# Kernel tuning notes

Hardware: AMD Instinct MI355X
Metric: run time of the kernel (lower is better)

Reference implementation:

```python
import jax, jax.numpy as jnp
import numpy as np

N_SEGMENTS = 512  # number of superpoint segments (range of sptids)


def setup_inputs() -> dict:
    key = jax.random.key(0)
    k1, k2, k3, k4 = jax.random.split(key, 4)
    n, m, c = 32768, 16384, 21
    points = jax.random.normal(k1, (n, 3), dtype=jnp.float32)
    scores = jax.random.normal(k2, (n, c), dtype=jnp.float32)
    d_points = jax.random.normal(k3, (m, 3), dtype=jnp.float32)
    sptids = jax.random.randint(k4, (m,), 0, N_SEGMENTS, dtype=jnp.int32)
    return {"points": points, "scores": scores, "d_points": d_points, "sptids": sptids}


def reference(points, scores, d_points, sptids):
    # --- brute-force nearest neighbor for ALL downsampled points at once ---
    # squared euclidean distance; argmin is identical to torch.cdist's argmin
    d2 = (jnp.sum(d_points * d_points, axis=1, keepdims=True)
          + jnp.sum(points * points, axis=1)[None, :]
          - 2.0 * (d_points @ points.T))          # [m, n]
    nn_idx = jnp.argmin(d2, axis=1)               # [m]
    gathered = scores[nn_idx]                     # [m, C] == assign_features output

    # --- per-segment mean of gathered scores, then argmax -> segment label ---
    seg_sum = jax.ops.segment_sum(gathered, sptids, num_segments=N_SEGMENTS)  # [S, C]
    counts = jax.ops.segment_sum(jnp.ones(sptids.shape, gathered.dtype), sptids,
                                 num_segments=N_SEGMENTS)                      # [S]
    seg_mean = seg_sum / jnp.maximum(counts, 1.0)[:, None]
    seg_labels = jnp.argmax(seg_mean, axis=1)     # [S]
    labels = seg_labels[sptids][:, None].astype(jnp.int32)  # [m, 1], original index order

    # torch.cat of seg_points over sorted unique ids == stable sort of d_points by sptid
    order = jnp.argsort(sptids, stable=True)
    new_points = d_points[order]                  # [m, 3]
    return new_points, labels
```

## Files before the change

### kernel.cpp

```cpp
#include <hip/hip_runtime.h>
#include <cfloat>
#include <cstdint>

#define NSEG 512
#define C 21
#define PPB 512
#define EPS_PICK 1e-3f

typedef _Float16 half8 __attribute__((ext_vector_type(8)));
typedef float f32x16 __attribute__((ext_vector_type(16)));

__global__ __launch_bounds__(256, 4)
void k1_mfma_scatter(const float* __restrict__ pts, const float* __restrict__ dpts,
                     const int* __restrict__ sptids,
                     float4* __restrict__ pts4, float* __restrict__ pbvT,
                     int* __restrict__ segbase, int* __restrict__ sorted_orig,
                     float* __restrict__ out, int n, int m, int NCH)
{
    __shared__ half8 lbuf[1024];
    const int bid = blockIdx.x, t = threadIdx.x;

    if (bid < NCH) {
        int sb = bid;
        int* Hb   = (int*)lbuf;
        int* Ht   = Hb + NSEG;
        int* pair = Ht + NSEG;
        int* segs = pair + 256;
        Hb[t] = 0; Hb[t + 256] = 0; Ht[t] = 0; Ht[t + 256] = 0;
        __syncthreads();
        int before = sb * 256;
        for (int idx = t; idx < m; idx += 256) {
            int s = sptids[idx];
            atomicAdd(&Ht[s], 1);
            if (idx < before) atomicAdd(&Hb[s], 1);
        }
        __syncthreads();
        int e0 = Ht[2 * t], e1 = Ht[2 * t + 1];
        int v = e0 + e1;
        pair[t] = v;
        __syncthreads();
        for (int off = 1; off < 256; off <<= 1) {
            int add = (t >= off) ? pair[t - off] : 0;
            __syncthreads();
            v += add; pair[t] = v;
            __syncthreads();
        }
        int prev = (t > 0) ? pair[t - 1] : 0;
        int b0 = prev, b1 = prev + e0;
        if (sb == 0) { segbase[2 * t] = b0; segbase[2 * t + 1] = b1; }
        int hb0 = Hb[2 * t], hb1 = Hb[2 * t + 1];
        __syncthreads();
        Hb[2 * t] = b0 + hb0;
        Hb[2 * t + 1] = b1 + hb1;
        int i = sb * 256 + t;
        segs[t] = (i < m) ? sptids[i] : -1;
        __syncthreads();
        if (i < m) {
            int seg = segs[t];
            int rank = 0;
            for (int j = 0; j < t; j++) rank += (segs[j] == seg) ? 1 : 0;
            int pos = Hb[seg] + rank;
            out[pos * 3 + 0] = dpts[i * 3 + 0];
            out[pos * 3 + 1] = dpts[i * 3 + 1];
            out[pos * 3 + 2] = dpts[i * 3 + 2];
            sorted_orig[pos] = i;
        }
        return;
    }

    const int b2 = bid - NCH;
    const int qb = b2 & 31, pc = b2 >> 5;
    const int wave = t >> 6, lane = t & 63;
    const int g = lane >> 5, col = lane & 31;

    half8 bq[4];
#pragma unroll
    for (int k = 0; k < 4; k++) {
        int q = (qb * 16 + wave * 4 + k) * 32 + col;
        float b0 = dpts[q * 3 + 0], b1 = dpts[q * 3 + 1], b2c = dpts[q * 3 + 2];
        _Float16 bh0 = (_Float16)b0; _Float16 bl0 = (_Float16)(b0 - (float)bh0);
        _Float16 bh1 = (_Float16)b1; _Float16 bl1 = (_Float16)(b1 - (float)bh1);
        _Float16 bh2 = (_Float16)b2c; _Float16 bl2 = (_Float16)(b2c - (float)bh2);
        const _Float16 one = (_Float16)1.f, zz = (_Float16)0.f;
        half8 g0 = {bh0, bl0, bh0, bh1, bl1, bh1, bh2, bl2};
        half8 g1 = {bh2, one, one, zz, zz, zz, zz, zz};
        bq[k] = g ? g1 : g0;
    }

#pragma unroll
    for (int half = 0; half < 2; half++) {
        int j = half * 256 + t;
        int i = pc * PPB + j;
        float x = pts[i * 3 + 0], y = pts[i * 3 + 1], z = pts[i * 3 + 2];
        if (qb == 0)
            pts4[i] = make_float4(x, y, z, fmaf(x, x, fmaf(y, y, z * z)));
        float a0 = -2.f * x, a1 = -2.f * y, a2 = -2.f * z;
        _Float16 ah0 = (_Float16)a0; _Float16 al0 = (_Float16)(a0 - (float)ah0);
        _Float16 ah1 = (_Float16)a1; _Float16 al1 = (_Float16)(a1 - (float)ah1);
        _Float16 ah2 = (_Float16)a2; _Float16 al2 = (_Float16)(a2 - (float)ah2);
        double ps = (double)x * x + (double)y * y + (double)z * z;
        _Float16 s0 = (_Float16)(float)ps;
        double r1 = ps - (double)(float)s0;
        _Float16 s1 = (_Float16)(float)r1;
        half8 g0 = {ah0, ah0, al0, ah1, ah1, al1, ah2, ah2};
        half8 g1 = {al2, s0, s1, (_Float16)0.f, (_Float16)0.f,
                    (_Float16)0.f, (_Float16)0.f, (_Float16)0.f};
        int base = (j >> 5) * 64 + (j & 31) * 2;
        lbuf[base + 0] = g0;
        lbuf[base + 1] = g1;
    }
    __syncthreads();

    float run0 = FLT_MAX, run1 = FLT_MAX, run2 = FLT_MAX, run3 = FLT_MAX;
    const f32x16 zero = {0.f,0.f,0.f,0.f,0.f,0.f,0.f,0.f,0.f,0.f,0.f,0.f,0.f,0.f,0.f,0.f};
    const int aoff = col * 2 + g;

#pragma unroll 4
    for (int tt = 0; tt < 16; tt++) {
        half8 a = lbuf[tt * 64 + aoff];
        f32x16 c0 = __builtin_amdgcn_mfma_f32_32x32x16_f16(a, bq[0], zero, 0, 0, 0);
        f32x16 c1 = __builtin_amdgcn_mfma_f32_32x32x16_f16(a, bq[1], zero, 0, 0, 0);
        f32x16 c2 = __builtin_amdgcn_mfma_f32_32x32x16_f16(a, bq[2], zero, 0, 0, 0);
        f32x16 c3 = __builtin_amdgcn_mfma_f32_32x32x16_f16(a, bq[3], zero, 0, 0, 0);
#define FOLD(cc, rr)  { \
        float v = fminf(fminf(cc[0], cc[1]), cc[2]);   \
        v = fminf(fminf(v, cc[3]), cc[4]);             \
        v = fminf(fminf(v, cc[5]), cc[6]);             \
        v = fminf(fminf(v, cc[7]), cc[8]);             \
        v = fminf(fminf(v, cc[9]), cc[10]);            \
        v = fminf(fminf(v, cc[11]), cc[12]);           \
        v = fminf(fminf(v, cc[13]), cc[14]);           \
        rr = fminf(fminf(v, cc[15]), rr); }
        FOLD(c0, run0) FOLD(c1, run1) FOLD(c2, run2) FOLD(c3, run3)
#undef FOLD
    }

    {
        int qbase = (qb * 512 + wave * 128) * 64;
        float v0 = fminf(run0, __shfl_xor(run0, 32, 64));
        float v1 = fminf(run1, __shfl_xor(run1, 32, 64));
        float v2 = fminf(run2, __shfl_xor(run2, 32, 64));
        float v3 = fminf(run3, __shfl_xor(run3, 32, 64));
        if (lane < 32) {
            pbvT[(size_t)qbase + (0 * 32 + lane) * 64 + pc] = v0;
            pbvT[(size_t)qbase + (1 * 32 + lane) * 64 + pc] = v1;
            pbvT[(size_t)qbase + (2 * 32 + lane) * 64 + pc] = v2;
            pbvT[(size_t)qbase + (3 * 32 + lane) * 64 + pc] = v3;
        }
    }
}

__global__ __launch_bounds__(1024)
void k2_seg_pick(const float4* __restrict__ pts4, const float* __restrict__ dpts,
                 const float* __restrict__ scores, const float* __restrict__ pbvT,
                 const int* __restrict__ segbase, const int* __restrict__ sorted_orig,
                 float* __restrict__ out, int n, int m)
{
    __shared__ double wsum[16][C];
    __shared__ double total[C];
    __shared__ float lab;
    const int t = threadIdx.x, wave = t >> 6, lane = t & 63;
    const int s = blockIdx.x;
    const int base = segbase[s];
    const int end  = (s == NSEG - 1) ? m : segbase[s + 1];

    double acc = 0.0;
    for (int j = base + wave; j < end; j += 16) {
        int q = sorted_orig[j];
        float myv = pbvT[(size_t)q * 64 + lane];
        float g1 = myv;
#pragma unroll
        for (int off = 1; off < 64; off <<= 1) g1 = fminf(g1, __shfl_xor(g1, off, 64));
        float thr = g1 + EPS_PICK;
        unsigned long long msk = __ballot(myv <= thr);

        float fx = dpts[q * 3 + 0], fy = dpts[q * 3 + 1], fz = dpts[q * 3 + 2];
        float fm2x = -2.f * fx, fm2y = -2.f * fy, fm2z = -2.f * fz;
        double m2x = -2.0 * (double)fx, m2y = -2.0 * (double)fy, m2z = -2.0 * (double)fz;
        double best = 1e308; int bi = 0x7fffffff;
        while (msk) {
            int pc = __builtin_ctzll(msk); msk &= msk - 1;
            int pbase = pc * PPB + lane;
#pragma unroll
            for (int r2 = 0; r2 < PPB / 64; r2++) {
                int i = pbase + r2 * 64;
                if (i < n) {
                    float4 p = pts4[i];
                    float v = fmaf(p.x, fm2x, fmaf(p.y, fm2y, fmaf(p.z, fm2z, p.w)));
                    if (v <= thr) {
                        double ps = (double)p.x * p.x + (double)p.y * p.y + (double)p.z * p.z;
                        double dv = fma((double)p.x, m2x, fma((double)p.y, m2y,
                                    fma((double)p.z, m2z, ps)));
                        if (dv < best || (dv == best && i < bi)) { best = dv; bi = i; }
                    }
                }
            }
        }
#pragma unroll
        for (int off = 32; off; off >>= 1) {
            double ov = __shfl_down(best, off, 64);
            int oi = __shfl_down(bi, off, 64);
            if (ov < best || (ov == best && oi < bi)) { best = ov; bi = oi; }
        }
        int bi0 = __shfl(bi, 0, 64);
        if (lane < C)
            acc += (double)scores[(size_t)bi0 * C + lane];
    }
    if (lane < C) wsum[wave][lane] = acc;
    __syncthreads();
    if (t < C) {
        double tv = 0.0;
#pragma unroll
        for (int w = 0; w < 16; w++) tv += wsum[w][t];
        total[t] = tv;
    }
    __syncthreads();
    if (t == 0) {
        double bv = total[0]; int best = 0;
        for (int c = 1; c < C; c++)
            if (total[c] > bv) { bv = total[c]; best = c; }
        lab = (float)best;
    }
    __syncthreads();
    float fb = lab;
    for (int j = base + t; j < end; j += 1024)
        out[(size_t)m * 3 + sorted_orig[j]] = fb;
}

extern "C" void kernel_launch(void* const* d_in, const int* in_sizes, int n_in,
                              void* d_out, int out_size, void* d_ws, size_t ws_size,
                              hipStream_t stream) {
    const float* points = (const float*)d_in[0];
    const float* scores = (const float*)d_in[1];
    const float* dpts   = (const float*)d_in[2];
    const int*   sptids = (const int*)d_in[3];

    int n = in_sizes[0] / 3;
    int m = in_sizes[2] / 3;
    int NCH   = (m + 255) / 256;
    int QB    = (m + 511) / 512;
    int PCg   = (n + 511) / 512;
    int MFMAB = QB * PCg;

    char* ws = (char*)d_ws;
    float4* pts4        = (float4*)ws;  ws += (size_t)n * sizeof(float4);
    float*  pbvT        = (float*)ws;   ws += (size_t)m * 64 * sizeof(float);
    int*    segbase     = (int*)ws;     ws += (size_t)NSEG * sizeof(int);
    int*    sorted_orig = (int*)ws;     ws += (size_t)m * sizeof(int);

    k1_mfma_scatter<<<NCH + MFMAB, 256, 0, stream>>>(points, dpts, sptids,
                                                     pts4, pbvT, segbase, sorted_orig,
                                                     (float*)d_out, n, m, NCH);
    k2_seg_pick<<<NSEG, 1024, 0, stream>>>(pts4, dpts, scores, pbvT,
                                           segbase, sorted_orig, (float*)d_out, n, m);
}
```

Baseline: 49.11 us.

## Track best and second-best MFMA tile per chunk to narrow exact rescoring

```diff
diff --git a/kernel.cpp b/kernel.cpp
--- a/kernel.cpp
+++ b/kernel.cpp
@@ -6,6 +6,7 @@
 #define C 21
 #define PPB 512
 #define EPS_PICK 1e-3f
+#define SLACK 1.5e-4f
 
 typedef _Float16 half8 __attribute__((ext_vector_type(8)));
 typedef float f32x16 __attribute__((ext_vector_type(16)));
@@ -14,6 +15,7 @@
 void k1_mfma_scatter(const float* __restrict__ pts, const float* __restrict__ dpts,
                      const int* __restrict__ sptids,
                      float4* __restrict__ pts4, float* __restrict__ pbvT,
+                     unsigned* __restrict__ auxT,
                      int* __restrict__ segbase, int* __restrict__ sorted_orig,
                      float* __restrict__ out, int n, int m, int NCH)
 {
@@ -111,7 +113,10 @@
     }
     __syncthreads();
 
-    float run0 = FLT_MAX, run1 = FLT_MAX, run2 = FLT_MAX, run3 = FLT_MAX;
+    float run1[4], run2[4];
+    int ttix[4];
+#pragma unroll
+    for (int k = 0; k < 4; k++) { run1[k] = FLT_MAX; run2[k] = FLT_MAX; ttix[k] = 0; }
     const f32x16 zero = {0.f,0.f,0.f,0.f,0.f,0.f,0.f,0.f,0.f,0.f,0.f,0.f,0.f,0.f,0.f,0.f};
     const int aoff = col * 2 + g;
 
@@ -122,7 +127,7 @@
         f32x16 c1 = __builtin_amdgcn_mfma_f32_32x32x16_f16(a, bq[1], zero, 0, 0, 0);
         f32x16 c2 = __builtin_amdgcn_mfma_f32_32x32x16_f16(a, bq[2], zero, 0, 0, 0);
         f32x16 c3 = __builtin_amdgcn_mfma_f32_32x32x16_f16(a, bq[3], zero, 0, 0, 0);
-#define FOLD(cc, rr)  { \
+#define FOLD(cc, kk)  { \
         float v = fminf(fminf(cc[0], cc[1]), cc[2]);   \
         v = fminf(fminf(v, cc[3]), cc[4]);             \
         v = fminf(fminf(v, cc[5]), cc[6]);             \
@@ -130,22 +135,32 @@
         v = fminf(fminf(v, cc[9]), cc[10]);            \
         v = fminf(fminf(v, cc[11]), cc[12]);           \
         v = fminf(fminf(v, cc[13]), cc[14]);           \
-        rr = fminf(fminf(v, cc[15]), rr); }
-        FOLD(c0, run0) FOLD(c1, run1) FOLD(c2, run2) FOLD(c3, run3)
+        v = fminf(v, cc[15]);                          \
+        float nr2 = fminf(run2[kk], fmaxf(v, run1[kk])); \
+        if (v < run1[kk]) { ttix[kk] = tt; run1[kk] = v; } \
+        run2[kk] = nr2; }
+        FOLD(c0, 0) FOLD(c1, 1) FOLD(c2, 2) FOLD(c3, 3)
 #undef FOLD
     }
 
-    {
-        int qbase = (qb * 512 + wave * 128) * 64;
-        float v0 = fminf(run0, __shfl_xor(run0, 32, 64));
-        float v1 = fminf(run1, __shfl_xor(run1, 32, 64));
-        float v2 = fminf(run2, __shfl_xor(run2, 32, 64));
-        float v3 = fminf(run3, __shfl_xor(run3, 32, 64));
+#pragma unroll
+    for (int k = 0; k < 4; k++) {
+        float o1 = __shfl_xor(run1[k], 32, 64);
+        float o2 = __shfl_xor(run2[k], 32, 64);
+        int   ot = __shfl_xor(ttix[k], 32, 64);
+        float lo1 = (lane < 32) ? run1[k] : o1;  int loT = (lane < 32) ? ttix[k] : ot;
+        float lo2 = (lane < 32) ? run2[k] : o2;
+        float hi1 = (lane < 32) ? o1 : run1[k];  int hiT = (lane < 32) ? ot : ttix[k];
+        float hi2 = (lane < 32) ? o2 : run2[k];
+        float r1c = fminf(lo1, hi1);
+        int Tstar = (lo1 <= hi1) ? loT : hiT;
+        float cl = (loT != Tstar) ? lo1 : lo2;
+        float ch = (hiT != Tstar) ? hi1 : hi2;
+        float L = fminf(cl, ch);
         if (lane < 32) {
-            pbvT[(size_t)qbase + (0 * 32 + lane) * 64 + pc] = v0;
-            pbvT[(size_t)qbase + (1 * 32 + lane) * 64 + pc] = v1;
-            pbvT[(size_t)qbase + (2 * 32 + lane) * 64 + pc] = v2;
-            pbvT[(size_t)qbase + (3 * 32 + lane) * 64 + pc] = v3;
+            size_t qi = (size_t)(qb * 512 + wave * 128 + k * 32 + lane) * 64 + pc;
+            pbvT[qi] = r1c;
+            auxT[qi] = (__float_as_uint(L) & ~0xFu) | (unsigned)Tstar;
         }
     }
 }
@@ -153,6 +168,7 @@
 __global__ __launch_bounds__(1024)
 void k2_seg_pick(const float4* __restrict__ pts4, const float* __restrict__ dpts,
                  const float* __restrict__ scores, const float* __restrict__ pbvT,
+                 const unsigned* __restrict__ auxT,
                  const int* __restrict__ segbase, const int* __restrict__ sorted_orig,
                  float* __restrict__ out, int n, int m)
 {
@@ -180,18 +196,37 @@
         double best = 1e308; int bi = 0x7fffffff;
         while (msk) {
             int pc = __builtin_ctzll(msk); msk &= msk - 1;
-            int pbase = pc * PPB + lane;
-#pragma unroll
-            for (int r2 = 0; r2 < PPB / 64; r2++) {
-                int i = pbase + r2 * 64;
-                if (i < n) {
-                    float4 p = pts4[i];
-                    float v = fmaf(p.x, fm2x, fmaf(p.y, fm2y, fmaf(p.z, fm2z, p.w)));
-                    if (v <= thr) {
-                        double ps = (double)p.x * p.x + (double)p.y * p.y + (double)p.z * p.z;
-                        double dv = fma((double)p.x, m2x, fma((double)p.y, m2y,
-                                    fma((double)p.z, m2z, ps)));
-                        if (dv < best || (dv == best && i < bi)) { best = dv; bi = i; }
+            unsigned au = auxT[(size_t)q * 64 + pc];
+            float L = __uint_as_float(au & ~0xFu);
+            int Ts = (int)(au & 0xFu);
+            if (L > thr + SLACK) {
+                if (lane < 32) {
+                    int i = pc * PPB + Ts * 32 + lane;
+                    if (i < n) {
+                        float4 p = pts4[i];
+                        float v = fmaf(p.x, fm2x, fmaf(p.y, fm2y, fmaf(p.z, fm2z, p.w)));
+                        if (v <= thr) {
+                            double ps = (double)p.x * p.x + (double)p.y * p.y + (double)p.z * p.z;
+                            double dv = fma((double)p.x, m2x, fma((double)p.y, m2y,
+                                        fma((double)p.z, m2z, ps)));
+                            if (dv < best || (dv == best && i < bi)) { best = dv; bi = i; }
+                        }
+                    }
+                }
+            } else {
+                int pbase = pc * PPB + lane;
+#pragma unroll
+                for (int r2 = 0; r2 < PPB / 64; r2++) {
+                    int i = pbase + r2 * 64;
+                    if (i < n) {
+                        float4 p = pts4[i];
+                        float v = fmaf(p.x, fm2x, fmaf(p.y, fm2y, fmaf(p.z, fm2z, p.w)));
+                        if (v <= thr) {
+                            double ps = (double)p.x * p.x + (double)p.y * p.y + (double)p.z * p.z;
+                            double dv = fma((double)p.x, m2x, fma((double)p.y, m2y,
+                                        fma((double)p.z, m2z, ps)));
+                            if (dv < best || (dv == best && i < bi)) { best = dv; bi = i; }
+                        }
                     }
                 }
             }
@@ -243,14 +278,15 @@
     int MFMAB = QB * PCg;
 
     char* ws = (char*)d_ws;
-    float4* pts4        = (float4*)ws;  ws += (size_t)n * sizeof(float4);
-    float*  pbvT        = (float*)ws;   ws += (size_t)m * 64 * sizeof(float);
-    int*    segbase     = (int*)ws;     ws += (size_t)NSEG * sizeof(int);
-    int*    sorted_orig = (int*)ws;     ws += (size_t)m * sizeof(int);
+    float4*   pts4        = (float4*)ws;    ws += (size_t)n * sizeof(float4);
+    float*    pbvT        = (float*)ws;     ws += (size_t)m * 64 * sizeof(float);
+    unsigned* auxT        = (unsigned*)ws;  ws += (size_t)m * 64 * sizeof(unsigned);
+    int*      segbase     = (int*)ws;       ws += (size_t)NSEG * sizeof(int);
+    int*      sorted_orig = (int*)ws;       ws += (size_t)m * sizeof(int);
 
     k1_mfma_scatter<<<NCH + MFMAB, 256, 0, stream>>>(points, dpts, sptids,
-                                                     pts4, pbvT, segbase, sorted_orig,
-                                                     (float*)d_out, n, m, NCH);
-    k2_seg_pick<<<NSEG, 1024, 0, stream>>>(pts4, dpts, scores, pbvT,
+                                                     pts4, pbvT, auxT, segbase,
+                                                     sorted_orig, (float*)d_out, n, m, NCH);
+    k2_seg_pick<<<NSEG, 1024, 0, stream>>>(pts4, dpts, scores, pbvT, auxT,
                                            segbase, sorted_orig, (float*)d_out, n, m);
 }
```

Measured after the change: 47.08 us. 1.04x faster.
